# Kernel optimization log

Measured on AMD Instinct MI355X. Metric: run time of the kernel, lower is better.

The kernel has to match this reference:

```python
import jax, jax.numpy as jnp
import numpy as np

B, T, D = 8, 512, 512
MAX_DUR = 15          # durations drawn from [0,16) then clamped to >=1
MAX_LEN = T * MAX_DUR # static padded frame length (torch pads to per-batch max)


def setup_inputs() -> dict:
    key = jax.random.key(0)
    kf, kd = jax.random.split(key)
    features = jax.random.normal(kf, (B, T, D), dtype=jnp.float32)
    durations = jax.random.randint(kd, (B, T), 0, 16, dtype=jnp.int32)
    return {"features": features, "durations": durations}


def reference(features, durations):
    """Duration-based length regulation (variable-length expand + pad).

    For each batch b, phoneme t is repeated durations[b,t] times along the
    frame axis; sequences are zero-padded to MAX_LEN. Implemented as a
    vectorized cumsum + searchsorted gather (no per-element host syncs).
    """
    Bv, Tv, Dv = features.shape
    dur = jnp.maximum(durations, 1)               # clamp(min=1) as in forward()
    cum = jnp.cumsum(dur, axis=1)                 # (B, T) exclusive-right frame boundaries
    pos = jnp.arange(MAX_LEN, dtype=cum.dtype)    # (MAX_LEN,)
    # idx[b, n] = source phoneme for output frame n: count of boundaries <= n
    idx = jax.vmap(lambda c: jnp.searchsorted(c, pos, side="right"))(cum)  # (B, MAX_LEN)
    valid = pos[None, :] < cum[:, -1:]            # (B, MAX_LEN) frames within total length
    idx = jnp.minimum(idx, Tv - 1)                # keep gather in-bounds for padded frames
    out = jnp.take_along_axis(features, idx[..., None], axis=1)  # (B, MAX_LEN, D)
    return jnp.where(valid[..., None], out, jnp.zeros((), features.dtype))
```

## Files before the change

kernel.cpp:

```cpp
#include <hip/hip_runtime.h>

#define BB 8
#define TT 512
#define DD 512
#define MAX_LEN 7680
#define FPB 30
#define BPB (MAX_LEN / FPB)

__global__ __launch_bounds__(256) void regulate_kernel(
    const float4* __restrict__ feat,
    const int2*   __restrict__ dur2,
    float4*       __restrict__ out)
{
    __shared__ int cum[TT];
    __shared__ int ps[256];

    const int t    = threadIdx.x;
    const int b    = blockIdx.x / BPB;
    const int base = (blockIdx.x % BPB) * FPB;

    int2 dd = dur2[b * (TT / 2) + t];
    int d0 = dd.x < 1 ? 1 : dd.x;
    int d1 = dd.y < 1 ? 1 : dd.y;
    ps[t] = d0 + d1;
    __syncthreads();
#pragma unroll
    for (int off = 1; off < 256; off <<= 1) {
        int x = (t >= off) ? ps[t - off] : 0;
        __syncthreads();
        ps[t] += x;
        __syncthreads();
    }
    int incl = ps[t];
    cum[2 * t]     = incl - d1;
    cum[2 * t + 1] = incl;
    __syncthreads();

    const int total = cum[TT - 1];
    const int lane  = t & 127;
    const int sub   = t >> 7;

#pragma unroll
    for (int j = 0; j < FPB; j += 2) {
        const int n = base + j + sub;
        float4 val = make_float4(0.f, 0.f, 0.f, 0.f);
        if (n < total) {
            int lo = 0, hi = TT;
#pragma unroll
            for (int s = 0; s < 10; ++s) {
                int mid = (lo + hi) >> 1;
                if (cum[mid] <= n) lo = mid + 1; else hi = mid;
            }
            val = feat[(size_t)(b * TT + lo) * (DD / 4) + lane];
        }
        out[((size_t)b * MAX_LEN + n) * (DD / 4) + lane] = val;
    }
}

extern "C" void kernel_launch(void* const* d_in, const int* in_sizes, int n_in,
                              void* d_out, int out_size, void* d_ws, size_t ws_size,
                              hipStream_t stream) {
    const float* feat;
    const int*   dur;
    if (in_sizes[0] == BB * TT) {
        dur  = (const int*)d_in[0];
        feat = (const float*)d_in[1];
    } else {
        feat = (const float*)d_in[0];
        dur  = (const int*)d_in[1];
    }
    float* out = (float*)d_out;

    regulate_kernel<<<BB * BPB, 256, 0, stream>>>(
        (const float4*)feat, (const int2*)dur, (float4*)out);
}
```

Measured before the change: 145.1 us.

## Walk frames sequentially per thread group with one search and nontemporal stores

Each half-block now handles a contiguous run of 15 frames. It runs a single binary search for the first frame, then advances the source phoneme index incrementally and reloads features only when the phoneme changes. Output writes use nontemporal stores, meant to avoid polluting the cache with the large write-only output. This cuts the repeated binary searches and redundant feature loads, but serialises the frame loop on a data-dependent chain. The per-frame store pattern also changes from interleaved to contiguous per half-block.

```diff
diff --git a/kernel.cpp b/kernel.cpp
--- a/kernel.cpp
+++ b/kernel.cpp
@@ -4,13 +4,16 @@
 #define TT 512
 #define DD 512
 #define MAX_LEN 7680
+#define FPG 15
 #define FPB 30
 #define BPB (MAX_LEN / FPB)
 
+typedef float vfloat4 __attribute__((ext_vector_type(4)));
+
 __global__ __launch_bounds__(256) void regulate_kernel(
-    const float4* __restrict__ feat,
-    const int2*   __restrict__ dur2,
-    float4*       __restrict__ out)
+    const vfloat4* __restrict__ feat,
+    const int2*    __restrict__ dur2,
+    vfloat4*       __restrict__ out)
 {
     __shared__ int cum[TT];
     __shared__ int ps[256];
@@ -39,21 +42,37 @@
     const int total = cum[TT - 1];
     const int lane  = t & 127;
     const int sub   = t >> 7;
+    const int n0    = base + sub * FPG;
+
+    int lo = 0;
+    {
+        int hi = TT;
+#pragma unroll
+        for (int s = 0; s < 10; ++s) {
+            int mid = (lo + hi) >> 1;
+            if (cum[mid] <= n0) lo = mid + 1; else hi = mid;
+        }
+    }
+    vfloat4 zero = {0.f, 0.f, 0.f, 0.f};
+    vfloat4 cur  = zero;
+    if (n0 < total)
+        cur = feat[(size_t)(b * TT + lo) * (DD / 4) + lane];
 
 #pragma unroll
-    for (int j = 0; j < FPB; j += 2) {
-        const int n = base + j + sub;
-        float4 val = make_float4(0.f, 0.f, 0.f, 0.f);
-        if (n < total) {
-            int lo = 0, hi = TT;
-#pragma unroll
-            for (int s = 0; s < 10; ++s) {
-                int mid = (lo + hi) >> 1;
-                if (cum[mid] <= n) lo = mid + 1; else hi = mid;
+    for (int i = 0; i < FPG; ++i) {
+        const int n = n0 + i;
+        if (i > 0) {
+            if (n < total) {
+                if (cum[lo] <= n) {
+                    ++lo;
+                    cur = feat[(size_t)(b * TT + lo) * (DD / 4) + lane];
+                }
+            } else {
+                cur = zero;
             }
-            val = feat[(size_t)(b * TT + lo) * (DD / 4) + lane];
         }
-        out[((size_t)b * MAX_LEN + n) * (DD / 4) + lane] = val;
+        __builtin_nontemporal_store(cur,
+            &out[((size_t)b * MAX_LEN + n) * (DD / 4) + lane]);
     }
 }
 
@@ -72,5 +91,5 @@
     float* out = (float*)d_out;
 
     regulate_kernel<<<BB * BPB, 256, 0, stream>>>(
-        (const float4*)feat, (const int2*)dur, (float4*)out);
+        (const vfloat4*)feat, (const int2*)dur, (vfloat4*)out);
 }
```

Result: no change. 145.1 us (+0.0%).
